# Kernel optimization log

Hardware: AMD Instinct MI355X
Metric: run time of the kernel (lower is better)

## Reference

```python
import jax, jax.numpy as jnp
import numpy as np

DMIN, DMAX = -1.0, 1.0
B, I, O, K = 1024, 256, 256, 128

def setup_inputs() -> dict:
    key = jax.random.key(0)
    k1, k2, k3 = jax.random.split(key, 3)
    x = jax.random.normal(k1, (B, I), dtype=jnp.float32)
    bound = 1.0 / np.sqrt(I)
    base_weight = jax.random.uniform(k2, (O, I), dtype=jnp.float32, minval=-bound, maxval=bound)
    coeff = 0.03 * jax.random.normal(k3, (O, I, K), dtype=jnp.float32)
    coeff = coeff - coeff.mean(axis=-1, keepdims=True)
    return {
        'x': x,
        'base_weight': base_weight,
        'spline_coefficients': coeff,
        'spline_scale': jnp.ones((O, I), dtype=jnp.float32),
        'bias': jnp.zeros((O,), dtype=jnp.float32),
    }


def reference(x, base_weight, spline_coefficients, spline_scale, bias):
    num_knots = spline_coefficients.shape[-1]
    step = (DMAX - DMIN) / (num_knots - 1)
    # input activation (tanh) then clamp to spline domain
    p = jnp.tanh(x)                                   # (B, I)
    c = jnp.clip(p, DMIN, DMAX)
    scaled = (c - DMIN) / step                        # in [0, K-1]
    left = jnp.clip(jnp.floor(scaled).astype(jnp.int32), 0, num_knots - 1)
    right = jnp.minimum(left + 1, num_knots - 1)
    frac = scaled - left.astype(p.dtype)              # (B, I)
    # fold spline_scale into coefficients, then gather only the 2 relevant knots
    Cs = spline_coefficients * spline_scale[..., None]  # (O, I, K)
    ii = jnp.arange(x.shape[1])[None, :]                # (1, I) broadcasts with (B, I)
    cl = Cs[:, ii, left]                                # (O, B, I)
    cr = Cs[:, ii, right]                               # (O, B, I)
    spline = jnp.einsum('bi,obi->bo', 1.0 - frac, cl) + jnp.einsum('bi,obi->bo', frac, cr)
    base = jax.nn.silu(p) @ base_weight.T               # (B, O)
    return base + spline + bias[None, :]
```

## Files before the change

kernel.cpp:

```cpp
#include <hip/hip_runtime.h>

constexpr int Bb = 1024;
constexpr int Ii = 256;
constexpr int Oo = 256;
constexpr int Kk = 128;
constexpr int NCH = 8;

typedef unsigned short u16;
typedef unsigned int u32;
typedef u16 ushort4v __attribute__((ext_vector_type(4)));
typedef float f4v __attribute__((ext_vector_type(4)));

__device__ __forceinline__ float bf16u_to_f(u16 u) {
    union { u32 ui; float f; } c;
    c.ui = ((u32)u) << 16;
    return c.f;
}
__device__ __forceinline__ u16 f_to_bf16(float f) {
    union { float f; u32 u; } c; c.f = f;
    u32 r = c.u + 0x7fffu + ((c.u >> 16) & 1u);
    return (u16)(r >> 16);
}

__global__ __launch_bounds__(256) void kperm(const float* __restrict__ cs,
                                             const float* __restrict__ scale,
                                             const float* __restrict__ wbase,
                                             u16* __restrict__ cp,
                                             float* __restrict__ wt) {
    __shared__ u16 T[128 * 66];
    int blk = blockIdx.x;
    int chunk = blk & 7;
    int sub = blk >> 3;
    int i  = chunk * 32 + (sub & 31);
    int oh = (sub >> 5) & 1, kh = (sub >> 6) & 1;
    int o0 = oh << 7, kb = kh << 6;
    int t = threadIdx.x;

    {
        int c4 = t & 15;
        int rb = t >> 4;
        const f4v* cs4 = (const f4v*)cs;
#pragma unroll
        for (int p = 0; p < 8; ++p) {
            int r = p * 16 + rb;
            int o = o0 + r;
            float sc = scale[o * Ii + i];
            f4v val = __builtin_nontemporal_load(
                &cs4[(size_t)(o * Ii + i) * (Kk / 4) + kh * 16 + c4]);
            int kl = c4 * 4;
            T[r * 66 + kl + 0] = f_to_bf16(val.x * sc);
            T[r * 66 + kl + 1] = f_to_bf16(val.y * sc);
            T[r * 66 + kl + 2] = f_to_bf16(val.z * sc);
            T[r * 66 + kl + 3] = f_to_bf16(val.w * sc);
        }
    }
    __syncthreads();
    {
        int og = t & 63;
        int kg = t >> 6;
#pragma unroll
        for (int m = 0; m < 16; ++m) {
            int kl = kg * 16 + m;
            u32 lo = T[(og * 2) * 66 + kl];
            u32 hi = T[(og * 2 + 1) * 66 + kl];
            *(u32*)&cp[((size_t)i * Kk + kb + kl) * Oo + o0 + og * 2] = lo | (hi << 16);
        }
    }
    if (blk < 256) {
        int gid = blk * 256 + t;
        wt[gid] = __builtin_nontemporal_load(&wbase[(gid & 255) * Ii + (gid >> 8)]);
    }
}

__global__ __launch_bounds__(256, 4) void kmain(const float* __restrict__ x,
                                                const char* __restrict__ cpb,
                                                const float* __restrict__ wt,
                                                float4* __restrict__ part4) {
    __shared__ float4 sf[256];
    __shared__ float wbuf[32 * 256];
    int t = threadIdx.x;
    int blk = blockIdx.x;
    int chunk = blk & (NCH - 1);
    int b0 = (blk >> 3) << 3;
    int i0 = chunk << 5;

    {
        int il = t & 31, bl = t >> 5;
        float xv = __builtin_nontemporal_load(
            &x[(size_t)(b0 + bl) * Ii + i0 + il]);
        float e2 = __expf(2.f * xv);
        float p = 1.f - 2.f / (e2 + 1.f);
        float s = p / (1.f + __expf(-p));
        float c = fminf(fmaxf(p, -1.f), 1.f);
        float scaled = (c + 1.f) * ((float)(Kk - 1) * 0.5f);
        int l = (int)floorf(scaled);
        l = min(max(l, 0), Kk - 1);
        int rr = min(l + 1, Kk - 1);
        float4 v;
        v.x = scaled - (float)l;
        v.y = s;
        v.z = __int_as_float(l * (Oo * 2));
        v.w = __int_as_float(rr * (Oo * 2));
        sf[il * 8 + bl] = v;
    }
    {
        const float4* wsrc4 = (const float4*)(wt + (size_t)i0 * Oo);
        float4* wb4 = (float4*)wbuf;
#pragma unroll
        for (int p = 0; p < 8; ++p)
            wb4[t + p * 256] = wsrc4[t + p * 256];
    }
    __syncthreads();

    int oq = t & 63;
    int bq = t >> 6;

    float a00=0.f,a01=0.f,a02=0.f,a03=0.f;
    float a10=0.f,a11=0.f,a12=0.f,a13=0.f;
    const char* cbase = cpb + (size_t)i0 * (Kk * Oo * 2) + oq * 8;

#pragma unroll 4
    for (int m = 0; m < 32; ++m) {
        float4 v0 = sf[m * 8 + bq * 2];
        float4 v1 = sf[m * 8 + bq * 2 + 1];
        float4 w = *(const float4*)&wbuf[m * 256 + oq * 4];
        const char* ci = cbase + (size_t)m * (Kk * Oo * 2);
        ushort4v cl0 = *(const ushort4v*)(ci + __float_as_int(v0.z));
        ushort4v cr0 = *(const ushort4v*)(ci + __float_as_int(v0.w));
        ushort4v cl1 = *(const ushort4v*)(ci + __float_as_int(v1.z));
        ushort4v cr1 = *(const ushort4v*)(ci + __float_as_int(v1.w));
        float f0 = v0.x, g0 = 1.f - v0.x, s0 = v0.y;
        float f1 = v1.x, g1 = 1.f - v1.x, s1 = v1.y;
        a00 = fmaf(s0, w.x, a00); a01 = fmaf(s0, w.y, a01);
        a02 = fmaf(s0, w.z, a02); a03 = fmaf(s0, w.w, a03);
        a10 = fmaf(s1, w.x, a10); a11 = fmaf(s1, w.y, a11);
        a12 = fmaf(s1, w.z, a12); a13 = fmaf(s1, w.w, a13);
        a00 = fmaf(g0, bf16u_to_f(cl0.x), a00); a00 = fmaf(f0, bf16u_to_f(cr0.x), a00);
        a01 = fmaf(g0, bf16u_to_f(cl0.y), a01); a01 = fmaf(f0, bf16u_to_f(cr0.y), a01);
        a02 = fmaf(g0, bf16u_to_f(cl0.z), a02); a02 = fmaf(f0, bf16u_to_f(cr0.z), a02);
        a03 = fmaf(g0, bf16u_to_f(cl0.w), a03); a03 = fmaf(f0, bf16u_to_f(cr0.w), a03);
        a10 = fmaf(g1, bf16u_to_f(cl1.x), a10); a10 = fmaf(f1, bf16u_to_f(cr1.x), a10);
        a11 = fmaf(g1, bf16u_to_f(cl1.y), a11); a11 = fmaf(f1, bf16u_to_f(cr1.y), a11);
        a12 = fmaf(g1, bf16u_to_f(cl1.z), a12); a12 = fmaf(f1, bf16u_to_f(cr1.z), a12);
        a13 = fmaf(g1, bf16u_to_f(cl1.w), a13); a13 = fmaf(f1, bf16u_to_f(cr1.w), a13);
    }

    size_t cstride = (size_t)(Bb * Oo / 4);
    float4 r0; r0.x=a00; r0.y=a01; r0.z=a02; r0.w=a03;
    float4 r1; r1.x=a10; r1.y=a11; r1.z=a12; r1.w=a13;
    part4[chunk * cstride + (size_t)(b0 + bq * 2) * (Oo / 4) + oq] = r0;
    part4[chunk * cstride + (size_t)(b0 + bq * 2 + 1) * (Oo / 4) + oq] = r1;
}

__global__ __launch_bounds__(256) void kreduce(const float4* __restrict__ part4,
                                               const float4* __restrict__ bias4,
                                               float4* __restrict__ out4) {
    int gid = blockIdx.x * 256 + threadIdx.x;
    const f4v* p = (const f4v*)(part4 + gid);
    f4v s = __builtin_nontemporal_load(p);
#pragma unroll
    for (int c = 1; c < NCH; ++c) {
        f4v v = __builtin_nontemporal_load(p + (size_t)c * (Bb * Oo / 4));
        s.x += v.x; s.y += v.y; s.z += v.z; s.w += v.w;
    }
    float4 bv = bias4[gid & 63];
    float4 o;
    o.x = s.x + bv.x; o.y = s.y + bv.y; o.z = s.z + bv.z; o.w = s.w + bv.w;
    out4[gid] = o;
}

extern "C" void kernel_launch(void* const* d_in, const int* in_sizes, int n_in,
                              void* d_out, int out_size, void* d_ws, size_t ws_size,
                              hipStream_t stream) {
    const float* x     = (const float*)d_in[0];
    const float* wbase = (const float*)d_in[1];
    const float* coeff = (const float*)d_in[2];
    const float* scale = (const float*)d_in[3];
    const float* bias  = (const float*)d_in[4];
    float* out = (float*)d_out;

    char* ws = (char*)d_ws;
    u16*    cp    = (u16*)ws;
    float*  wt    = (float*)(ws + (16u << 20));
    float4* part4 = (float4*)(ws + (17u << 20));

    kperm<<<1024, 256, 0, stream>>>(coeff, scale, wbase, cp, wt);
    kmain<<<1024, 256, 0, stream>>>(x, (const char*)cp, wt, part4);
    kreduce<<<(Bb * Oo / 4) / 256, 256, 0, stream>>>(part4, (const float4*)bias, (float4*)out);
}
```

Before: 110.1 us.

## Fuse split-I reduction into main kernel via last-block atomic counter; widen loads

Removes the separate reduce kernel. Each block in kmain bumps an atomic counter for its batch tile, and the last of the eight chunk blocks sums the partials, adds the bias and writes the output. The counter is reset inside kperm. Each thread now owns 8 outputs for one batch row and gathers 16-byte bf16 vectors instead of two 8-byte vectors for two rows, which changes the shape of the memory access. Together these save one launch and aim for wider gathers, at the cost of a thread fence and an atomic per block.

```diff
diff --git a/kernel.cpp b/kernel.cpp
--- a/kernel.cpp
+++ b/kernel.cpp
@@ -8,7 +8,7 @@
 
 typedef unsigned short u16;
 typedef unsigned int u32;
-typedef u16 ushort4v __attribute__((ext_vector_type(4)));
+typedef u16 ushort8v __attribute__((ext_vector_type(8)));
 typedef float f4v __attribute__((ext_vector_type(4)));
 
 __device__ __forceinline__ float bf16u_to_f(u16 u) {
@@ -26,7 +26,8 @@
                                              const float* __restrict__ scale,
                                              const float* __restrict__ wbase,
                                              u16* __restrict__ cp,
-                                             float* __restrict__ wt) {
+                                             float* __restrict__ wt,
+                                             int* __restrict__ cnt) {
     __shared__ u16 T[128 * 66];
     int blk = blockIdx.x;
     int chunk = blk & 7;
@@ -70,18 +71,25 @@
         int gid = blk * 256 + t;
         wt[gid] = __builtin_nontemporal_load(&wbase[(gid & 255) * Ii + (gid >> 8)]);
     }
+    if (blk == 512 && t < 128) cnt[t] = 0;
 }
 
 __global__ __launch_bounds__(256, 4) void kmain(const float* __restrict__ x,
                                                 const char* __restrict__ cpb,
                                                 const float* __restrict__ wt,
-                                                float4* __restrict__ part4) {
+                                                float4* __restrict__ part4,
+                                                int* __restrict__ cnt,
+                                                const float4* __restrict__ bias4,
+                                                float4* __restrict__ out4) {
     __shared__ float4 sf[256];
-    __shared__ float wbuf[32 * 256];
+    __shared__ float4 wA[32 * 32];
+    __shared__ float4 wB[32 * 32];
+    __shared__ int lastFlag;
     int t = threadIdx.x;
     int blk = blockIdx.x;
     int chunk = blk & (NCH - 1);
-    int b0 = (blk >> 3) << 3;
+    int bt = blk >> 3;
+    int b0 = bt << 3;
     int i0 = chunk << 5;
 
     {
@@ -104,69 +112,76 @@
         sf[il * 8 + bl] = v;
     }
     {
-        const float4* wsrc4 = (const float4*)(wt + (size_t)i0 * Oo);
-        float4* wb4 = (float4*)wbuf;
-#pragma unroll
-        for (int p = 0; p < 8; ++p)
-            wb4[t + p * 256] = wsrc4[t + p * 256];
+        int j = t & 31, mr = t >> 5;
+#pragma unroll
+        for (int p = 0; p < 4; ++p) {
+            int m = p * 8 + mr;
+            const float* src = wt + (size_t)(i0 + m) * Oo + j * 8;
+            wA[m * 32 + j] = *(const float4*)(src);
+            wB[m * 32 + j] = *(const float4*)(src + 4);
+        }
     }
     __syncthreads();
 
-    int oq = t & 63;
-    int bq = t >> 6;
-
-    float a00=0.f,a01=0.f,a02=0.f,a03=0.f;
-    float a10=0.f,a11=0.f,a12=0.f,a13=0.f;
-    const char* cbase = cpb + (size_t)i0 * (Kk * Oo * 2) + oq * 8;
+    int oq = t & 31;
+    int bl = t >> 5;
+    float a0=0.f,a1=0.f,a2=0.f,a3=0.f,a4=0.f,a5=0.f,a6=0.f,a7=0.f;
+    const char* cbase = cpb + (size_t)i0 * (Kk * Oo * 2) + oq * 16;
 
 #pragma unroll 4
     for (int m = 0; m < 32; ++m) {
-        float4 v0 = sf[m * 8 + bq * 2];
-        float4 v1 = sf[m * 8 + bq * 2 + 1];
-        float4 w = *(const float4*)&wbuf[m * 256 + oq * 4];
+        float4 v = sf[m * 8 + bl];
+        float4 wa = wA[m * 32 + oq];
+        float4 wb = wB[m * 32 + oq];
         const char* ci = cbase + (size_t)m * (Kk * Oo * 2);
-        ushort4v cl0 = *(const ushort4v*)(ci + __float_as_int(v0.z));
-        ushort4v cr0 = *(const ushort4v*)(ci + __float_as_int(v0.w));
-        ushort4v cl1 = *(const ushort4v*)(ci + __float_as_int(v1.z));
-        ushort4v cr1 = *(const ushort4v*)(ci + __float_as_int(v1.w));
-        float f0 = v0.x, g0 = 1.f - v0.x, s0 = v0.y;
-        float f1 = v1.x, g1 = 1.f - v1.x, s1 = v1.y;
-        a00 = fmaf(s0, w.x, a00); a01 = fmaf(s0, w.y, a01);
-        a02 = fmaf(s0, w.z, a02); a03 = fmaf(s0, w.w, a03);
-        a10 = fmaf(s1, w.x, a10); a11 = fmaf(s1, w.y, a11);
-        a12 = fmaf(s1, w.z, a12); a13 = fmaf(s1, w.w, a13);
-        a00 = fmaf(g0, bf16u_to_f(cl0.x), a00); a00 = fmaf(f0, bf16u_to_f(cr0.x), a00);
-        a01 = fmaf(g0, bf16u_to_f(cl0.y), a01); a01 = fmaf(f0, bf16u_to_f(cr0.y), a01);
-        a02 = fmaf(g0, bf16u_to_f(cl0.z), a02); a02 = fmaf(f0, bf16u_to_f(cr0.z), a02);
-        a03 = fmaf(g0, bf16u_to_f(cl0.w), a03); a03 = fmaf(f0, bf16u_to_f(cr0.w), a03);
-        a10 = fmaf(g1, bf16u_to_f(cl1.x), a10); a10 = fmaf(f1, bf16u_to_f(cr1.x), a10);
-        a11 = fmaf(g1, bf16u_to_f(cl1.y), a11); a11 = fmaf(f1, bf16u_to_f(cr1.y), a11);
-        a12 = fmaf(g1, bf16u_to_f(cl1.z), a12); a12 = fmaf(f1, bf16u_to_f(cr1.z), a12);
-        a13 = fmaf(g1, bf16u_to_f(cl1.w), a13); a13 = fmaf(f1, bf16u_to_f(cr1.w), a13);
+        ushort8v cl = *(const ushort8v*)(ci + __float_as_int(v.z));
+        ushort8v cr = *(const ushort8v*)(ci + __float_as_int(v.w));
+        float f = v.x, g = 1.f - v.x, s = v.y;
+        a0 = fmaf(s, wa.x, a0); a1 = fmaf(s, wa.y, a1);
+        a2 = fmaf(s, wa.z, a2); a3 = fmaf(s, wa.w, a3);
+        a4 = fmaf(s, wb.x, a4); a5 = fmaf(s, wb.y, a5);
+        a6 = fmaf(s, wb.z, a6); a7 = fmaf(s, wb.w, a7);
+        a0 = fmaf(g, bf16u_to_f(cl[0]), a0); a0 = fmaf(f, bf16u_to_f(cr[0]), a0);
+        a1 = fmaf(g, bf16u_to_f(cl[1]), a1); a1 = fmaf(f, bf16u_to_f(cr[1]), a1);
+        a2 = fmaf(g, bf16u_to_f(cl[2]), a2); a2 = fmaf(f, bf16u_to_f(cr[2]), a2);
+        a3 = fmaf(g, bf16u_to_f(cl[3]), a3); a3 = fmaf(f, bf16u_to_f(cr[3]), a3);
+        a4 = fmaf(g, bf16u_to_f(cl[4]), a4); a4 = fmaf(f, bf16u_to_f(cr[4]), a4);
+        a5 = fmaf(g, bf16u_to_f(cl[5]), a5); a5 = fmaf(f, bf16u_to_f(cr[5]), a5);
+        a6 = fmaf(g, bf16u_to_f(cl[6]), a6); a6 = fmaf(f, bf16u_to_f(cr[6]), a6);
+        a7 = fmaf(g, bf16u_to_f(cl[7]), a7); a7 = fmaf(f, bf16u_to_f(cr[7]), a7);
     }
 
     size_t cstride = (size_t)(Bb * Oo / 4);
-    float4 r0; r0.x=a00; r0.y=a01; r0.z=a02; r0.w=a03;
-    float4 r1; r1.x=a10; r1.y=a11; r1.z=a12; r1.w=a13;
-    part4[chunk * cstride + (size_t)(b0 + bq * 2) * (Oo / 4) + oq] = r0;
-    part4[chunk * cstride + (size_t)(b0 + bq * 2 + 1) * (Oo / 4) + oq] = r1;
-}
-
-__global__ __launch_bounds__(256) void kreduce(const float4* __restrict__ part4,
-                                               const float4* __restrict__ bias4,
-                                               float4* __restrict__ out4) {
-    int gid = blockIdx.x * 256 + threadIdx.x;
-    const f4v* p = (const f4v*)(part4 + gid);
-    f4v s = __builtin_nontemporal_load(p);
-#pragma unroll
-    for (int c = 1; c < NCH; ++c) {
-        f4v v = __builtin_nontemporal_load(p + (size_t)c * (Bb * Oo / 4));
-        s.x += v.x; s.y += v.y; s.z += v.z; s.w += v.w;
-    }
-    float4 bv = bias4[gid & 63];
-    float4 o;
-    o.x = s.x + bv.x; o.y = s.y + bv.y; o.z = s.z + bv.z; o.w = s.w + bv.w;
-    out4[gid] = o;
+    {
+        float4 r0; r0.x=a0; r0.y=a1; r0.z=a2; r0.w=a3;
+        float4 r1; r1.x=a4; r1.y=a5; r1.z=a6; r1.w=a7;
+        size_t pb = (size_t)chunk * cstride + (size_t)(b0 + bl) * (Oo / 4) + oq * 2;
+        part4[pb]     = r0;
+        part4[pb + 1] = r1;
+    }
+
+    __threadfence();
+    if (t == 0) lastFlag = (atomicAdd(&cnt[bt], 1) == NCH - 1);
+    __syncthreads();
+    if (lastFlag) {
+        __threadfence();
+#pragma unroll
+        for (int q = 0; q < 2; ++q) {
+            int gid = bt * 512 + q * 256 + t;
+            const f4v* p = (const f4v*)(part4 + gid);
+            f4v s4 = __builtin_nontemporal_load(p);
+#pragma unroll
+            for (int c = 1; c < NCH; ++c) {
+                f4v vv = __builtin_nontemporal_load(p + (size_t)c * cstride);
+                s4.x += vv.x; s4.y += vv.y; s4.z += vv.z; s4.w += vv.w;
+            }
+            float4 bv = bias4[gid & 63];
+            float4 o;
+            o.x = s4.x + bv.x; o.y = s4.y + bv.y;
+            o.z = s4.z + bv.z; o.w = s4.w + bv.w;
+            out4[gid] = o;
+        }
+    }
 }
 
 extern "C" void kernel_launch(void* const* d_in, const int* in_sizes, int n_in,
@@ -177,14 +192,15 @@
     const float* coeff = (const float*)d_in[2];
     const float* scale = (const float*)d_in[3];
     const float* bias  = (const float*)d_in[4];
-    float* out = (float*)d_out;
+    float4* out4 = (float4*)d_out;
 
     char* ws = (char*)d_ws;
     u16*    cp    = (u16*)ws;
     float*  wt    = (float*)(ws + (16u << 20));
+    int*    cnt   = (int*)(ws + (16u << 20) + (512u << 10));
     float4* part4 = (float4*)(ws + (17u << 20));
 
-    kperm<<<1024, 256, 0, stream>>>(coeff, scale, wbase, cp, wt);
-    kmain<<<1024, 256, 0, stream>>>(x, (const char*)cp, wt, part4);
-    kreduce<<<(Bb * Oo / 4) / 256, 256, 0, stream>>>(part4, (const float4*)bias, (float4*)out);
-}
+    kperm<<<1024, 256, 0, stream>>>(coeff, scale, wbase, cp, wt, cnt);
+    kmain<<<1024, 256, 0, stream>>>(x, (const char*)cp, wt, part4, cnt,
+                                    (const float4*)bias, out4);
+}
```

Measured after the change: 292.5 us. 166% more time.
